# Kernel optimization log

Measured on AMD Instinct MI355X. Metric: run time of the kernel, lower is better.

Reference implementation:

```python
import jax, jax.numpy as jnp
import numpy as np

B, N, C = 2, 2048, 1024
H = 16
R = 4
MLP = 4096
LORA_SCALE = 1.0 / R  # lora_alpha=1, r=4
EPS = 1e-5


def _ln(x, g, b):
    m = jnp.mean(x, axis=-1, keepdims=True)
    v = jnp.mean(jnp.square(x - m), axis=-1, keepdims=True)
    return (x - m) * jax.lax.rsqrt(v + EPS) * g + b


def setup_inputs() -> dict:
    key = jax.random.key(0)
    ks = jax.random.split(key, 16)
    s = lambda k, shape, fan: jax.random.normal(k, shape, jnp.float32) * (1.0 / np.sqrt(fan))
    return {
        "x": jax.random.normal(ks[0], (B, N, C), jnp.float32),
        "pos": jax.random.normal(ks[1], (B, N, C), jnp.float32),
        "Wqkv": s(ks[2], (3 * C, C), C),
        "b_qkv": jnp.zeros((3 * C,), jnp.float32),
        "lora_A": s(ks[3], (2 * R, C), C),          # rows 0:R -> q, R:2R -> v
        "lora_B": s(ks[4], (2 * C, R), R) * 0.1,     # rows 0:C -> q, C:2C -> v
        "Wproj": s(ks[5], (C, C), C),
        "b_proj": jnp.zeros((C,), jnp.float32),
        "ln1_g": jnp.ones((C,), jnp.float32),
        "ln1_b": jnp.zeros((C,), jnp.float32),
        "ln2_g": jnp.ones((C,), jnp.float32),
        "ln2_b": jnp.zeros((C,), jnp.float32),
        "W1": s(ks[6], (MLP, C), C),
        "b1": jnp.zeros((MLP,), jnp.float32),
        "W2": s(ks[7], (C, MLP), MLP),
        "b2": jnp.zeros((C,), jnp.float32),
        "idx": 0,
    }


def reference(x, pos, Wqkv, b_qkv, lora_A, lora_B, Wproj, b_proj,
              ln1_g, ln1_b, ln2_g, ln2_b, W1, b1, W2, b2, idx):
    # (dropout layers are identity in eval mode)
    x = x + pos

    # --- attention block: Residual(PreNormDrop(SelfAttention)) ---
    h = _ln(x, ln1_g, ln1_b)                              # [B,N,C]
    qkv = h @ Wqkv.T + b_qkv                              # [B,N,3C]
    # LoRA MergedLinear: low-rank update on q and v thirds only
    after_A = h @ lora_A.T                                # [B,N,2R]
    dq = after_A[..., :R] @ lora_B[:C].T * LORA_SCALE     # [B,N,C]
    dv = after_A[..., R:] @ lora_B[C:].T * LORA_SCALE     # [B,N,C]
    qkv = qkv.at[..., :C].add(dq).at[..., 2 * C:].add(dv)

    Dh = C // H
    q, k, v = [t.reshape(B, N, H, Dh).transpose(0, 2, 1, 3)
               for t in jnp.split(qkv, 3, axis=-1)]       # each [B,H,N,Dh]
    scale = Dh ** -0.5
    attn = jnp.einsum('bhid,bhjd->bhij', q, k) * scale    # [B,H,N,N]
    attn = jax.nn.softmax(attn, axis=-1)
    o = jnp.einsum('bhij,bhjd->bhid', attn, v)            # [B,H,N,Dh]
    o = o.transpose(0, 2, 1, 3).reshape(B, N, C)
    o = o @ Wproj.T + b_proj
    x = x + o

    # --- FFN block: Residual(PreNorm(FeedForward)) ---
    h2 = _ln(x, ln2_g, ln2_b)
    h2 = jax.nn.gelu(h2 @ W1.T + b1, approximate=False)
    h2 = h2 @ W2.T + b2
    return x + h2
```

## Files before the change

### kernel.cpp

```cpp
#include <hip/hip_runtime.h>
#include <hip/hip_bf16.h>
#include <math.h>

typedef __hip_bfloat16 bf16;
typedef __attribute__((ext_vector_type(4))) float f32x4;
typedef __attribute__((ext_vector_type(16))) float f32x16;
typedef __attribute__((ext_vector_type(8))) short s16x8;

__device__ __forceinline__ void async_cp16(void* lds, const void* g) {
    __builtin_amdgcn_global_load_lds((const __attribute__((address_space(1))) void*)g,
                                     (__attribute__((address_space(3))) void*)lds, 16, 0, 0);
}

__device__ __forceinline__ float gelu_fast(float x) {
    float y = 1.5957691216f * (x + 0.044715f * x * x * x);
    float t = __expf(y);
    float th = 1.0f - 2.0f / (t + 1.0f);
    return 0.5f * x * (1.0f + th);
}

__global__ __launch_bounds__(256)
void cvt_all(const float* __restrict__ w0, const float* __restrict__ w1,
             const float* __restrict__ w2, const float* __restrict__ w3,
             bf16* __restrict__ o0, bf16* __restrict__ o1,
             bf16* __restrict__ o2, bf16* __restrict__ o3) {
    int i = blockIdx.x * 256 + threadIdx.x;
    const float* src; bf16* dst; int j = i;
    if (j < 786432)            { src = w0; dst = o0; }
    else if (j < 1048576)      { j -= 786432;  src = w1; dst = o1; }
    else if (j < 2097152)      { j -= 1048576; src = w2; dst = o2; }
    else                       { j -= 2097152; src = w3; dst = o3; }
    float4 v = ((const float4*)src)[j];
    union { bf16 o[4]; uint2 u; } pk;
    pk.o[0] = __float2bfloat16(v.x); pk.o[1] = __float2bfloat16(v.y);
    pk.o[2] = __float2bfloat16(v.z); pk.o[3] = __float2bfloat16(v.w);
    ((uint2*)dst)[j] = pk.u;
}

template <bool ADD>
__global__ __launch_bounds__(256)
void ln_kernel(const float* __restrict__ xin, const float* __restrict__ pos,
               const float* __restrict__ gam, const float* __restrict__ bet,
               float* __restrict__ x1, bf16* __restrict__ hout) {
    const int row = blockIdx.x, tid = threadIdx.x;
    const size_t off = (size_t)row * 1024;
    float4 v = ((const float4*)(xin + off))[tid];
    if constexpr (ADD) {
        float4 p = ((const float4*)(pos + off))[tid];
        v.x += p.x; v.y += p.y; v.z += p.z; v.w += p.w;
        ((float4*)(x1 + off))[tid] = v;
    }
    float s  = v.x + v.y + v.z + v.w;
    float s2 = v.x*v.x + v.y*v.y + v.z*v.z + v.w*v.w;
#pragma unroll
    for (int o = 32; o >= 1; o >>= 1) { s += __shfl_xor(s, o); s2 += __shfl_xor(s2, o); }
    __shared__ float sS[4], sS2[4];
    int w = tid >> 6, lane = tid & 63;
    if (lane == 0) { sS[w] = s; sS2[w] = s2; }
    __syncthreads();
    float mean = (sS[0] + sS[1] + sS[2] + sS[3]) * (1.f / 1024.f);
    float e2   = (sS2[0] + sS2[1] + sS2[2] + sS2[3]) * (1.f / 1024.f);
    float rstd = rsqrtf(e2 - mean * mean + 1e-5f);
    float4 gv = ((const float4*)gam)[tid], bv = ((const float4*)bet)[tid];
    bf16* ho = hout + off + tid * 4;
    ho[0] = __float2bfloat16((v.x - mean) * rstd * gv.x + bv.x);
    ho[1] = __float2bfloat16((v.y - mean) * rstd * gv.y + bv.y);
    ho[2] = __float2bfloat16((v.z - mean) * rstd * gv.z + bv.z);
    ho[3] = __float2bfloat16((v.w - mean) * rstd * gv.w + bv.w);
}

template <int MODE>
__global__ __launch_bounds__(256)
void gemm_bk64(const bf16* __restrict__ A, const bf16* __restrict__ B,
               const float* __restrict__ bias, bf16* __restrict__ outp,
               int M, int N, int K, int gx) {
    __shared__ bf16 As[2][128 * 64];
    __shared__ bf16 Bs[2][128 * 64];
    const int tid = threadIdx.x;
    const int lane = tid & 63, w = tid >> 6;
    const int grp = lane >> 4, c16 = lane & 15;
    const int wm = (w & 1) * 64, wn = (w >> 1) * 64;
    const int nwg = gridDim.x, bid = blockIdx.x;
    const int sw = (bid & 7) * (nwg >> 3) + (bid >> 3);
    const int bm = (sw / gx) * 128, bn = (sw % gx) * 128;

    f32x4 acc[4][4];
    const f32x4 zero = {0.f, 0.f, 0.f, 0.f};
#pragma unroll
    for (int mi = 0; mi < 4; mi++)
#pragma unroll
        for (int ni = 0; ni < 4; ni++) acc[mi][ni] = zero;

#define STAGE128(bufi, k0)                                                          \
    {                                                                               \
        const int buf_ = (bufi);                                                    \
        const int koff_ = (k0);                                                     \
        _Pragma("unroll") for (int t_ = 0; t_ < 4; t_++) {                          \
            int s_ = t_ * 256 + tid;                                                \
            int row_ = s_ >> 3, db_ = s_ & 7;                                       \
            int gb_ = (db_ ^ (row_ & 7)) << 3;                                      \
            async_cp16(&As[buf_][s_ * 8], A + (size_t)(bm + row_) * K + koff_ + gb_); \
            async_cp16(&Bs[buf_][s_ * 8], B + (size_t)(bn + row_) * K + koff_ + gb_); \
        }                                                                           \
    }

#define COMPUTE128(bufi)                                                            \
    {                                                                               \
        const int buf_ = (bufi);                                                    \
        _Pragma("unroll") for (int kc_ = 0; kc_ < 2; kc_++) {                       \
            s16x8 af_[4], bfv_[4];                                                  \
            _Pragma("unroll") for (int mi_ = 0; mi_ < 4; mi_++) {                   \
                int r_ = wm + mi_ * 16 + c16;                                       \
                af_[mi_] = *(const s16x8*)&As[buf_][r_ * 64 + ((((kc_ << 2) | grp) ^ (r_ & 7)) << 3)]; \
            }                                                                       \
            _Pragma("unroll") for (int ni_ = 0; ni_ < 4; ni_++) {                   \
                int r_ = wn + ni_ * 16 + c16;                                       \
                bfv_[ni_] = *(const s16x8*)&Bs[buf_][r_ * 64 + ((((kc_ << 2) | grp) ^ (r_ & 7)) << 3)]; \
            }                                                                       \
            _Pragma("unroll") for (int mi_ = 0; mi_ < 4; mi_++)                     \
                _Pragma("unroll") for (int ni_ = 0; ni_ < 4; ni_++)                 \
                    acc[mi_][ni_] = __builtin_amdgcn_mfma_f32_16x16x32_bf16(af_[mi_], bfv_[ni_], acc[mi_][ni_], 0, 0, 0); \
        }                                                                           \
    }

    STAGE128(0, 0);
    __syncthreads();
    const int nk = K >> 6;
    int cur = 0;
    for (int t = 0; t < nk - 1; t++) {
        STAGE128(cur ^ 1, (t + 1) << 6);
        COMPUTE128(cur);
        __syncthreads();
        cur ^= 1;
    }
    COMPUTE128(cur);

#undef STAGE128
#undef COMPUTE128

#pragma unroll
    for (int mi = 0; mi < 4; mi++)
#pragma unroll
        for (int ni = 0; ni < 4; ni++) {
            int r0 = bm + wm + mi * 16 + grp * 4;
            int c  = bn + wn + ni * 16 + c16;
            float bv = bias[c];
#pragma unroll
            for (int q = 0; q < 4; q++) {
                size_t idx = (size_t)(r0 + q) * N + c;
                float v = acc[mi][ni][q] + bv;
                if constexpr (MODE == 2) v = gelu_fast(v);
                outp[idx] = __float2bfloat16(v);
            }
        }
}

__global__ __launch_bounds__(256)
void gemm_n64(const bf16* __restrict__ A, const bf16* __restrict__ B,
              const float* __restrict__ bias, const float* __restrict__ resid,
              float* __restrict__ outp, int M, int N, int K, int gx) {
    __shared__ bf16 As[3][128 * 64];
    __shared__ bf16 Bs[3][64 * 64];
    const int tid = threadIdx.x;
    const int lane = tid & 63, w = tid >> 6;
    const int grp = lane >> 4, c16 = lane & 15;
    const int wm = w * 32;
    const int nwg = gridDim.x, bid = blockIdx.x;
    const int sw = (bid & 7) * (nwg >> 3) + (bid >> 3);
    const int bm = (sw / gx) * 128, bn = (sw % gx) * 64;

    f32x4 acc[2][4];
    const f32x4 zero = {0.f, 0.f, 0.f, 0.f};
#pragma unroll
    for (int mi = 0; mi < 2; mi++)
#pragma unroll
        for (int ni = 0; ni < 4; ni++) acc[mi][ni] = zero;

#define STAGE64(bufi, k0)                                                           \
    {                                                                               \
        const int buf_ = (bufi);                                                    \
        const int koff_ = (k0);                                                     \
        _Pragma("unroll") for (int t_ = 0; t_ < 4; t_++) {                          \
            int s_ = t_ * 256 + tid;                                                \
            int row_ = s_ >> 3, db_ = s_ & 7;                                       \
            async_cp16(&As[buf_][s_ * 8], A + (size_t)(bm + row_) * K + koff_ + ((db_ ^ (row_ & 7)) << 3)); \
        }                                                                           \
        _Pragma("unroll") for (int t_ = 0; t_ < 2; t_++) {                          \
            int s_ = t_ * 256 + tid;                                                \
            int row_ = s_ >> 3, db_ = s_ & 7;                                       \
            async_cp16(&Bs[buf_][s_ * 8], B + (size_t)(bn + row_) * K + koff_ + ((db_ ^ (row_ & 7)) << 3)); \
        }                                                                           \
    }

#define COMPUTE64(bufi)                                                             \
    {                                                                               \
        const int buf_ = (bufi);                                                    \
        _Pragma("unroll") for (int kc_ = 0; kc_ < 2; kc_++) {                       \
            s16x8 af_[2], bfv_[4];                                                  \
            _Pragma("unroll") for (int mi_ = 0; mi_ < 2; mi_++) {                   \
                int r_ = wm + mi_ * 16 + c16;                                       \
                af_[mi_] = *(const s16x8*)&As[buf_][r_ * 64 + ((((kc_ << 2) | grp) ^ (r_ & 7)) << 3)]; \
            }                                                                       \
            _Pragma("unroll") for (int ni_ = 0; ni_ < 4; ni_++) {                   \
                int rb_ = ni_ * 16 + c16;                                           \
                bfv_[ni_] = *(const s16x8*)&Bs[buf_][rb_ * 64 + ((((kc_ << 2) | grp) ^ (rb_ & 7)) << 3)]; \
            }                                                                       \
            _Pragma("unroll") for (int mi_ = 0; mi_ < 2; mi_++)                     \
                _Pragma("unroll") for (int ni_ = 0; ni_ < 4; ni_++)                 \
                    acc[mi_][ni_] = __builtin_amdgcn_mfma_f32_16x16x32_bf16(af_[mi_], bfv_[ni_], acc[mi_][ni_], 0, 0, 0); \
        }                                                                           \
    }

#define WAITV12 asm volatile("s_waitcnt vmcnt(12)" ::: "memory")
#define WAITV6  asm volatile("s_waitcnt vmcnt(6)"  ::: "memory")
#define WAITV0  asm volatile("s_waitcnt vmcnt(0)"  ::: "memory")

#define STEP64(BQ, TQ)                                                              \
    {                                                                               \
        const int tq_ = (TQ);                                                       \
        COMPUTE64(BQ);                                                              \
        __builtin_amdgcn_s_barrier();            \
        if (tq_ + 3 < nk) { STAGE64(BQ, (tq_ + 3) << 6); WAITV12; }                 \
        else if (tq_ + 2 < nk) { WAITV6; }                                          \
        else { WAITV0; }                                \
        __builtin_amdgcn_s_barrier();             \
    }

    const int nk = K >> 6;
    STAGE64(0, 0);
    STAGE64(1, 64);
    STAGE64(2, 128);
    WAITV12;
    __builtin_amdgcn_s_barrier();

    for (int t = 0; t < nk - 1; t += 3) {
        STEP64(0, t);
        STEP64(1, t + 1);
        STEP64(2, t + 2);
    }
    COMPUTE64(0);

#undef STEP64
#undef WAITV12
#undef WAITV6
#undef WAITV0
#undef STAGE64
#undef COMPUTE64

#pragma unroll
    for (int mi = 0; mi < 2; mi++)
#pragma unroll
        for (int ni = 0; ni < 4; ni++) {
            int r0 = bm + wm + mi * 16 + grp * 4;
            int c  = bn + ni * 16 + c16;
            float bv = bias[c];
#pragma unroll
            for (int q = 0; q < 4; q++) {
                size_t idx = (size_t)(r0 + q) * N + c;
                outp[idx] = acc[mi][ni][q] + bv + resid[idx];
            }
        }
}

__global__ __launch_bounds__(256)
void lora_a_kernel(const bf16* __restrict__ h, const float* __restrict__ A,
                   float* __restrict__ afterA) {
    const int row = blockIdx.x, tid = threadIdx.x;
    float hv[4];
#pragma unroll
    for (int t = 0; t < 4; t++) hv[t] = __bfloat162float(h[(size_t)row * 1024 + tid * 4 + t]);
    float p[8];
#pragma unroll
    for (int r = 0; r < 8; r++) {
        float4 av = ((const float4*)(A + (size_t)r * 1024))[tid];
        p[r] = hv[0] * av.x + hv[1] * av.y + hv[2] * av.z + hv[3] * av.w;
    }
#pragma unroll
    for (int r = 0; r < 8; r++)
#pragma unroll
        for (int o = 32; o >= 1; o >>= 1) p[r] += __shfl_xor(p[r], o);
    __shared__ float red[4][8];
    int w = tid >> 6, lane = tid & 63;
    if (lane == 0) {
#pragma unroll
        for (int r = 0; r < 8; r++) red[w][r] = p[r];
    }
    __syncthreads();
    if (tid < 8) afterA[(size_t)row * 8 + tid] = red[0][tid] + red[1][tid] + red[2][tid] + red[3][tid];
}

__global__ __launch_bounds__(256)
void attn_prep(const bf16* __restrict__ qkv, const float* __restrict__ afterA,
               const float* __restrict__ loraB, bf16* __restrict__ Qb,
               bf16* __restrict__ Kb, bf16* __restrict__ Vt) {
    const int bh = blockIdx.y, b = bh >> 4, h = bh & 15;
    const int it = blockIdx.x;
    __shared__ bf16 Vs[64 * 65];
    const int tid = threadIdx.x;
#pragma unroll
    for (int t = 0; t < 16; t++) {
        int s = t * 256 + tid;
        int il = s >> 6, d = s & 63;
        int ig = b * 2048 + it * 64 + il;
        size_t grow = (size_t)ig * 3072 + h * 64 + d;
        int col = h * 64 + d;
        const float* aA = afterA + (size_t)ig * 8;
        float4 bq = ((const float4*)loraB)[col];
        float4 bvv = ((const float4*)loraB)[1024 + col];
        float dq = (aA[0]*bq.x  + aA[1]*bq.y  + aA[2]*bq.z  + aA[3]*bq.w)  * 0.25f;
        float dv = (aA[4]*bvv.x + aA[5]*bvv.y + aA[6]*bvv.z + aA[7]*bvv.w) * 0.25f;
        float q = (__bfloat162float(qkv[grow]) + dq) * 0.18033688011f;
        float k = __bfloat162float(qkv[grow + 1024]);
        float v = __bfloat162float(qkv[grow + 2048]) + dv;
        size_t orow = (size_t)(bh * 2048 + it * 64 + il) * 64 + d;
        Qb[orow] = __float2bfloat16(q);
        Kb[orow] = __float2bfloat16(k);
        Vs[d * 65 + il] = __float2bfloat16(v);
    }
    __syncthreads();
#pragma unroll
    for (int t = 0; t < 16; t++) {
        int s = t * 256 + tid;
        int d = s >> 6, il = s & 63;
        Vt[(size_t)(bh * 64 + d) * 2048 + it * 64 + il] = Vs[d * 65 + il];
    }
}

__global__ __launch_bounds__(256)
void attn_fused(const bf16* __restrict__ Qb, const bf16* __restrict__ Kb,
                const bf16* __restrict__ Vt, bf16* __restrict__ Og) {
    __shared__ bf16 Qs[128 * 64], Ks[2][64 * 64], Vs[2][64 * 64];
    const int tid = threadIdx.x;
    const int lane = tid & 63, w = tid >> 6;
    const int c32 = lane & 31, l5 = lane >> 5;
    const int bid = blockIdx.x;
    const int sw = (bid & 7) * 64 + (bid >> 3);
    const int bh = sw >> 4, b = bh >> 4, h = bh & 15;
    const int i0 = (sw & 15) * 128;
    const int rowperm = (c32 & 19) | (((c32 >> 3) & 1) << 2) | (((c32 >> 2) & 1) << 3);

    const size_t qbase = (size_t)(bh * 2048 + i0) * 64;
    const size_t kbase = (size_t)bh * 2048 * 64;
    const size_t vbase = (size_t)bh * 64 * 2048;

#define STAGEKV(bufi, jv)                                                           \
    {                                                                               \
        const int buf_ = (bufi);                                                    \
        const int joff_ = (jv);                                                     \
        _Pragma("unroll") for (int t_ = 0; t_ < 2; t_++) {                          \
            int s_ = t_ * 256 + tid;                                                \
            int row_ = s_ >> 3, db_ = s_ & 7;                                       \
            int gb_ = (db_ ^ (row_ & 7)) << 3;                                      \
            async_cp16(&Ks[buf_][s_ * 8], Kb + kbase + (size_t)(joff_ + row_) * 64 + gb_); \
            async_cp16(&Vs[buf_][s_ * 8], Vt + vbase + (size_t)row_ * 2048 + joff_ + gb_); \
        }                                                                           \
    }

#pragma unroll
    for (int t = 0; t < 4; t++) {
        int s = t * 256 + tid;
        int row = s >> 3, db = s & 7;
        async_cp16(&Qs[s * 8], Qb + qbase + row * 64 + ((db ^ (row & 7)) << 3));
    }
    STAGEKV(0, 0);
    __syncthreads();

    s16x8 qf[4];
    {
        int rq = w * 32 + c32;
#pragma unroll
        for (int kc = 0; kc < 4; kc++) {
            int db = 2 * kc + l5;
            qf[kc] = *(const s16x8*)&Qs[rq * 64 + ((db ^ (rq & 7)) << 3)];
        }
    }

    f32x16 Oq[2];
#pragma unroll
    for (int dq = 0; dq < 2; dq++)
#pragma unroll
        for (int r = 0; r < 16; r++) Oq[dq][r] = 0.f;
    float l_lane = 0.f;

#define ATILE(BUF, JN)                                                              \
    {                                                                               \
        const int jn_ = (JN);                                                       \
        if (jn_ < 32) { STAGEKV((BUF) ^ 1, jn_ << 6); }                             \
        f32x16 Sq[2];                                                               \
        __builtin_amdgcn_s_setprio(1);                                              \
        _Pragma("unroll") for (int jq_ = 0; jq_ < 2; jq_++) {                       \
            _Pragma("unroll") for (int r_ = 0; r_ < 16; r_++) Sq[jq_][r_] = 0.f;    \
            int rk_ = jq_ * 32 + rowperm;                                           \
            _Pragma("unroll") for (int kc_ = 0; kc_ < 4; kc_++) {                   \
                int db_ = 2 * kc_ + l5;                                             \
                s16x8 af_ = *(const s16x8*)&Ks[BUF][rk_ * 64 + ((db_ ^ (rk_ & 7)) << 3)]; \
                Sq[jq_] = __builtin_amdgcn_mfma_f32_32x32x16_bf16(af_, qf[kc_], Sq[jq_], 0, 0, 0); \
            }                                                                       \
        }                                                                           \
        __builtin_amdgcn_s_setprio(0);                                              \
        s16x8 pf_[4];                                                               \
        _Pragma("unroll") for (int kc_ = 0; kc_ < 4; kc_++) {                       \
            union { s16x8 v; unsigned u4[4]; } u_;                                  \
            _Pragma("unroll") for (int pr_ = 0; pr_ < 4; pr_++) {                   \
                float a_ = Sq[kc_ >> 1][8 * (kc_ & 1) + 2 * pr_];                   \
                float b_ = Sq[kc_ >> 1][8 * (kc_ & 1) + 2 * pr_ + 1];               \
                float pa_, pb_;                                                     \
                asm("v_exp_f32 %0, %1" : "=v"(pa_) : "v"(a_));                      \
                asm("v_exp_f32 %0, %1" : "=v"(pb_) : "v"(b_));                      \
                l_lane += pa_; l_lane += pb_;                                       \
                unsigned pk_;                                                       \
                asm("v_cvt_pk_bf16_f32 %0, %1, %2" : "=v"(pk_) : "v"(pa_), "v"(pb_)); \
                u_.u4[pr_] = pk_;                                                   \
            }                                                                       \
            pf_[kc_] = u_.v;                                                        \
        }                                                                           \
        __builtin_amdgcn_s_setprio(1);                                              \
        _Pragma("unroll") for (int dq_ = 0; dq_ < 2; dq_++) {                       \
            int rd_ = dq_ * 32 + c32;                                               \
            _Pragma("unroll") for (int kc_ = 0; kc_ < 4; kc_++) {                   \
                int jb_ = 2 * kc_ + l5;                                             \
                s16x8 af_ = *(const s16x8*)&Vs[BUF][rd_ * 64 + ((jb_ ^ (rd_ & 7)) << 3)]; \
                Oq[dq_] = __builtin_amdgcn_mfma_f32_32x32x16_bf16(af_, pf_[kc_], Oq[dq_], 0, 0, 0); \
            }                                                                       \
        }                                                                           \
        __builtin_amdgcn_s_setprio(0);                                              \
        __syncthreads();                                                            \
    }

    for (int jt = 0; jt < 32; jt += 2) {
        ATILE(0, jt + 1);
        ATILE(1, jt + 2);
    }
#undef ATILE
#undef STAGEKV

    float l = l_lane + __shfl_xor(l_lane, 32);
    float inv = 1.0f / fmaxf(l, 1e-35f);
    int i = i0 + w * 32 + c32;
    size_t obase = (size_t)(b * 2048 + i) * 1024 + h * 64;
#pragma unroll
    for (int dq = 0; dq < 2; dq++)
#pragma unroll
        for (int rg = 0; rg < 4; rg++) {
            union { bf16 e[4]; uint2 u; } pk;
#pragma unroll
            for (int c = 0; c < 4; c++)
                pk.e[c] = __float2bfloat16(Oq[dq][rg * 4 + c] * inv);
            int d0 = dq * 32 + l5 * 4 + rg * 8;
            *(uint2*)&Og[obase + d0] = pk.u;
        }
}

extern "C" void kernel_launch(void* const* d_in, const int* in_sizes, int n_in,
                              void* d_out, int out_size, void* d_ws, size_t ws_size,
                              hipStream_t stream) {
    const float* x     = (const float*)d_in[0];
    const float* pos   = (const float*)d_in[1];
    const float* Wqkv  = (const float*)d_in[2];
    const float* bqkv  = (const float*)d_in[3];
    const float* loraA = (const float*)d_in[4];
    const float* loraB = (const float*)d_in[5];
    const float* Wproj = (const float*)d_in[6];
    const float* bproj = (const float*)d_in[7];
    const float* ln1g  = (const float*)d_in[8];
    const float* ln1b  = (const float*)d_in[9];
    const float* ln2g  = (const float*)d_in[10];
    const float* ln2b  = (const float*)d_in[11];
    const float* W1    = (const float*)d_in[12];
    const float* b1    = (const float*)d_in[13];
    const float* W2    = (const float*)d_in[14];
    const float* b2    = (const float*)d_in[15];

    char* ws = (char*)d_ws;
    float* x1     = (float*)(ws + 0);
    bf16*  hbuf   = (bf16*) (ws + 16777216);
    bf16*  qkv    = (bf16*) (ws + 25165824);
    bf16*  gbuf   = (bf16*) (ws + 50331648);
    float* afterA = (float*)(ws + 83886080);
    bf16*  Qb     = (bf16*) (ws + 84017152);
    bf16*  Kb     = (bf16*) (ws + 92405760);
    bf16*  Vt     = (bf16*) (ws + 100794368);
    bf16*  Obf    = (bf16*) (ws + 109182976);
    bf16*  Wqkvb  = (bf16*) (ws + 117571584);
    bf16*  Wprojb = (bf16*) (ws + 123863040);
    bf16*  W1b    = (bf16*) (ws + 125960192);
    bf16*  W2b    = (bf16*) (ws + 134348800);

    cvt_all<<<12288, 256, 0, stream>>>(Wqkv, Wproj, W1, W2, Wqkvb, Wprojb, W1b, W2b);

    ln_kernel<true><<<4096, 256, 0, stream>>>(x, pos, ln1g, ln1b, x1, hbuf);

    gemm_bk64<0><<<768, 256, 0, stream>>>(hbuf, Wqkvb, bqkv, qkv, 4096, 3072, 1024, 24);

    lora_a_kernel<<<4096, 256, 0, stream>>>(hbuf, loraA, afterA);

    attn_prep<<<dim3(32, 32), 256, 0, stream>>>(qkv, afterA, loraB, Qb, Kb, Vt);
    attn_fused<<<512, 256, 0, stream>>>(Qb, Kb, Vt, Obf);

    gemm_n64<<<512, 256, 0, stream>>>(Obf, Wprojb, bproj, x1, x1, 4096, 1024, 1024, 16);

    ln_kernel<false><<<4096, 256, 0, stream>>>(x1, nullptr, ln2g, ln2b, nullptr, hbuf);

    gemm_bk64<2><<<1024, 256, 0, stream>>>(hbuf, W1b, b1, gbuf, 4096, 4096, 1024, 32);

    gemm_n64<<<512, 256, 0, stream>>>(gbuf, W2b, b2, x1, (float*)d_out, 4096, 1024, 4096, 16);

    (void)in_sizes; (void)n_in; (void)out_size; (void)ws_size;
}
```

Before: 383.8 us.

## Triple-buffer bf16 GEMM with 512-thread blocks and explicit vmcnt waits

The QKV and FFN-up GEMM kernel now runs 8 waves per block, each covering a 64x32 sub-tile instead of 64x64, and cycles through three LDS stages instead of two. Loads are issued three tiles ahead, and explicit s_waitcnt vmcnt counts plus raw s_barrier replace the __syncthreads double-buffer loop. The goal is better hiding of global-to-LDS latency and more waves available to interleave MFMA work. In exchange, LDS use rises to 96KB per block, which likely caps each CU at one block, and each step now has two barriers.

```diff
diff --git a/kernel.cpp b/kernel.cpp
--- a/kernel.cpp
+++ b/kernel.cpp
@@ -70,33 +70,33 @@
 }
 
 template <int MODE>
-__global__ __launch_bounds__(256)
+__global__ __launch_bounds__(512)
 void gemm_bk64(const bf16* __restrict__ A, const bf16* __restrict__ B,
                const float* __restrict__ bias, bf16* __restrict__ outp,
                int M, int N, int K, int gx) {
-    __shared__ bf16 As[2][128 * 64];
-    __shared__ bf16 Bs[2][128 * 64];
+    __shared__ bf16 As[3][128 * 64];
+    __shared__ bf16 Bs[3][128 * 64];
     const int tid = threadIdx.x;
     const int lane = tid & 63, w = tid >> 6;
     const int grp = lane >> 4, c16 = lane & 15;
-    const int wm = (w & 1) * 64, wn = (w >> 1) * 64;
+    const int wm = (w & 1) * 64, wn = (w >> 1) * 32;
     const int nwg = gridDim.x, bid = blockIdx.x;
     const int sw = (bid & 7) * (nwg >> 3) + (bid >> 3);
     const int bm = (sw / gx) * 128, bn = (sw % gx) * 128;
 
-    f32x4 acc[4][4];
+    f32x4 acc[4][2];
     const f32x4 zero = {0.f, 0.f, 0.f, 0.f};
 #pragma unroll
     for (int mi = 0; mi < 4; mi++)
 #pragma unroll
-        for (int ni = 0; ni < 4; ni++) acc[mi][ni] = zero;
+        for (int ni = 0; ni < 2; ni++) acc[mi][ni] = zero;
 
 #define STAGE128(bufi, k0)                                                          \
     {                                                                               \
         const int buf_ = (bufi);                                                    \
         const int koff_ = (k0);                                                     \
-        _Pragma("unroll") for (int t_ = 0; t_ < 4; t_++) {                          \
-            int s_ = t_ * 256 + tid;                                                \
+        _Pragma("unroll") for (int t_ = 0; t_ < 2; t_++) {                          \
+            int s_ = t_ * 512 + tid;                                                \
             int row_ = s_ >> 3, db_ = s_ & 7;                                       \
             int gb_ = (db_ ^ (row_ & 7)) << 3;                                      \
             async_cp16(&As[buf_][s_ * 8], A + (size_t)(bm + row_) * K + koff_ + gb_); \
@@ -108,40 +108,61 @@
     {                                                                               \
         const int buf_ = (bufi);                                                    \
         _Pragma("unroll") for (int kc_ = 0; kc_ < 2; kc_++) {                       \
-            s16x8 af_[4], bfv_[4];                                                  \
+            s16x8 af_[4], bfv_[2];                                                  \
             _Pragma("unroll") for (int mi_ = 0; mi_ < 4; mi_++) {                   \
                 int r_ = wm + mi_ * 16 + c16;                                       \
                 af_[mi_] = *(const s16x8*)&As[buf_][r_ * 64 + ((((kc_ << 2) | grp) ^ (r_ & 7)) << 3)]; \
             }                                                                       \
-            _Pragma("unroll") for (int ni_ = 0; ni_ < 4; ni_++) {                   \
+            _Pragma("unroll") for (int ni_ = 0; ni_ < 2; ni_++) {                   \
                 int r_ = wn + ni_ * 16 + c16;                                       \
                 bfv_[ni_] = *(const s16x8*)&Bs[buf_][r_ * 64 + ((((kc_ << 2) | grp) ^ (r_ & 7)) << 3)]; \
             }                                                                       \
             _Pragma("unroll") for (int mi_ = 0; mi_ < 4; mi_++)                     \
-                _Pragma("unroll") for (int ni_ = 0; ni_ < 4; ni_++)                 \
+                _Pragma("unroll") for (int ni_ = 0; ni_ < 2; ni_++)                 \
                     acc[mi_][ni_] = __builtin_amdgcn_mfma_f32_16x16x32_bf16(af_[mi_], bfv_[ni_], acc[mi_][ni_], 0, 0, 0); \
         }                                                                           \
     }
 
+#define WAITV8 asm volatile("s_waitcnt vmcnt(8)" ::: "memory")
+#define WAITV4 asm volatile("s_waitcnt vmcnt(4)" ::: "memory")
+#define WAITV0 asm volatile("s_waitcnt vmcnt(0)" ::: "memory")
+
+#define STEP128(BQ, TQ)                                                             \
+    {                                                                               \
+        const int tq_ = (TQ);                                                       \
+        COMPUTE128(BQ);                                                             \
+        __builtin_amdgcn_s_barrier();            \
+        if (tq_ + 3 < nk) { STAGE128(BQ, (tq_ + 3) << 6); WAITV8; }                 \
+        else if (tq_ + 2 < nk) { WAITV4; }                                          \
+        else { WAITV0; }                                \
+        __builtin_amdgcn_s_barrier();             \
+    }
+
+    const int nk = K >> 6;
     STAGE128(0, 0);
-    __syncthreads();
-    const int nk = K >> 6;
-    int cur = 0;
-    for (int t = 0; t < nk - 1; t++) {
-        STAGE128(cur ^ 1, (t + 1) << 6);
-        COMPUTE128(cur);
-        __syncthreads();
-        cur ^= 1;
-    }
-    COMPUTE128(cur);
-
+    STAGE128(1, 64);
+    STAGE128(2, 128);
+    WAITV8;
+    __builtin_amdgcn_s_barrier();
+
+    for (int t = 0; t < nk - 1; t += 3) {
+        STEP128(0, t);
+        STEP128(1, t + 1);
+        STEP128(2, t + 2);
+    }
+    COMPUTE128(0);
+
+#undef STEP128
+#undef WAITV8
+#undef WAITV4
+#undef WAITV0
 #undef STAGE128
 #undef COMPUTE128
 
 #pragma unroll
     for (int mi = 0; mi < 4; mi++)
 #pragma unroll
-        for (int ni = 0; ni < 4; ni++) {
+        for (int ni = 0; ni < 2; ni++) {
             int r0 = bm + wm + mi * 16 + grp * 4;
             int c  = bn + wn + ni * 16 + c16;
             float bv = bias[c];
@@ -490,7 +511,7 @@
 
     ln_kernel<true><<<4096, 256, 0, stream>>>(x, pos, ln1g, ln1b, x1, hbuf);
 
-    gemm_bk64<0><<<768, 256, 0, stream>>>(hbuf, Wqkvb, bqkv, qkv, 4096, 3072, 1024, 24);
+    gemm_bk64<0><<<768, 512, 0, stream>>>(hbuf, Wqkvb, bqkv, qkv, 4096, 3072, 1024, 24);
 
     lora_a_kernel<<<4096, 256, 0, stream>>>(hbuf, loraA, afterA);
 
@@ -501,7 +522,7 @@
 
     ln_kernel<false><<<4096, 256, 0, stream>>>(x1, nullptr, ln2g, ln2b, nullptr, hbuf);
 
-    gemm_bk64<2><<<1024, 256, 0, stream>>>(hbuf, W1b, b1, gbuf, 4096, 4096, 1024, 32);
+    gemm_bk64<2><<<1024, 512, 0, stream>>>(hbuf, W1b, b1, gbuf, 4096, 4096, 1024, 32);
 
     gemm_n64<<<512, 256, 0, stream>>>(gbuf, W2b, b2, x1, (float*)d_out, 4096, 1024, 4096, 16);
 
```

Result: slower. 391.5 us (+2.0%).

## Enlarge bf16 GEMM tiles to 256x256 with 512 threads and deeper prefetch

Applied to the files above, without the earlier changes.

The bk64 GEMM used for the QKV projection and FFN1 now computes a 256x256 output tile per block with 8 waves, each wave owning a 128x64 sub-tile. The K loop is restructured so two 64-wide K tiles are kept in flight, using explicit vmcnt waits and raw barriers instead of a single-stage prefetch with __syncthreads. The aim is more operand reuse per LDS load and fewer global reloads of A and B. In exchange, LDS use grows to 128KB per block, so only one block fits per CU. Grids shrink to 192 and 256 blocks, which may leave some CUs idle on the QKV GEMM.

```diff
diff --git a/kernel.cpp b/kernel.cpp
--- a/kernel.cpp
+++ b/kernel.cpp
@@ -70,33 +70,33 @@
 }
 
 template <int MODE>
-__global__ __launch_bounds__(256)
+__global__ __launch_bounds__(512, 2)
 void gemm_bk64(const bf16* __restrict__ A, const bf16* __restrict__ B,
                const float* __restrict__ bias, bf16* __restrict__ outp,
                int M, int N, int K, int gx) {
-    __shared__ bf16 As[2][128 * 64];
-    __shared__ bf16 Bs[2][128 * 64];
+    __shared__ bf16 As[2][256 * 64];
+    __shared__ bf16 Bs[2][256 * 64];
     const int tid = threadIdx.x;
     const int lane = tid & 63, w = tid >> 6;
     const int grp = lane >> 4, c16 = lane & 15;
-    const int wm = (w & 1) * 64, wn = (w >> 1) * 64;
+    const int wm = (w & 1) * 128, wn = (w >> 1) * 64;
     const int nwg = gridDim.x, bid = blockIdx.x;
     const int sw = (bid & 7) * (nwg >> 3) + (bid >> 3);
-    const int bm = (sw / gx) * 128, bn = (sw % gx) * 128;
-
-    f32x4 acc[4][4];
+    const int bm = (sw / gx) * 256, bn = (sw % gx) * 256;
+
+    f32x4 acc[8][4];
     const f32x4 zero = {0.f, 0.f, 0.f, 0.f};
 #pragma unroll
-    for (int mi = 0; mi < 4; mi++)
+    for (int mi = 0; mi < 8; mi++)
 #pragma unroll
         for (int ni = 0; ni < 4; ni++) acc[mi][ni] = zero;
 
-#define STAGE128(bufi, k0)                                                          \
+#define STAGE256(bufi, k0)                                                          \
     {                                                                               \
         const int buf_ = (bufi);                                                    \
         const int koff_ = (k0);                                                     \
         _Pragma("unroll") for (int t_ = 0; t_ < 4; t_++) {                          \
-            int s_ = t_ * 256 + tid;                                                \
+            int s_ = t_ * 512 + tid;                                                \
             int row_ = s_ >> 3, db_ = s_ & 7;                                       \
             int gb_ = (db_ ^ (row_ & 7)) << 3;                                      \
             async_cp16(&As[buf_][s_ * 8], A + (size_t)(bm + row_) * K + koff_ + gb_); \
@@ -104,12 +104,12 @@
         }                                                                           \
     }
 
-#define COMPUTE128(bufi)                                                            \
+#define COMPUTE256(bufi)                                                            \
     {                                                                               \
         const int buf_ = (bufi);                                                    \
         _Pragma("unroll") for (int kc_ = 0; kc_ < 2; kc_++) {                       \
-            s16x8 af_[4], bfv_[4];                                                  \
-            _Pragma("unroll") for (int mi_ = 0; mi_ < 4; mi_++) {                   \
+            s16x8 af_[8], bfv_[4];                                                  \
+            _Pragma("unroll") for (int mi_ = 0; mi_ < 8; mi_++) {                   \
                 int r_ = wm + mi_ * 16 + c16;                                       \
                 af_[mi_] = *(const s16x8*)&As[buf_][r_ * 64 + ((((kc_ << 2) | grp) ^ (r_ & 7)) << 3)]; \
             }                                                                       \
@@ -117,29 +117,46 @@
                 int r_ = wn + ni_ * 16 + c16;                                       \
                 bfv_[ni_] = *(const s16x8*)&Bs[buf_][r_ * 64 + ((((kc_ << 2) | grp) ^ (r_ & 7)) << 3)]; \
             }                                                                       \
-            _Pragma("unroll") for (int mi_ = 0; mi_ < 4; mi_++)                     \
+            _Pragma("unroll") for (int mi_ = 0; mi_ < 8; mi_++)                     \
                 _Pragma("unroll") for (int ni_ = 0; ni_ < 4; ni_++)                 \
                     acc[mi_][ni_] = __builtin_amdgcn_mfma_f32_16x16x32_bf16(af_[mi_], bfv_[ni_], acc[mi_][ni_], 0, 0, 0); \
         }                                                                           \
     }
 
-    STAGE128(0, 0);
-    __syncthreads();
+#define WAITV8 asm volatile("s_waitcnt vmcnt(8)" ::: "memory")
+#define WAITV0 asm volatile("s_waitcnt vmcnt(0)" ::: "memory")
+
+#define STEP256(BQ, TQ)                                                             \
+    {                                                                               \
+        const int tq_ = (TQ);                                                       \
+        COMPUTE256(BQ);                                                             \
+        __builtin_amdgcn_s_barrier();            \
+        if (tq_ + 2 < nk) { STAGE256(BQ, (tq_ + 2) << 6); WAITV8; }                 \
+        else { WAITV0; }                                \
+        __builtin_amdgcn_s_barrier();             \
+    }
+
     const int nk = K >> 6;
-    int cur = 0;
-    for (int t = 0; t < nk - 1; t++) {
-        STAGE128(cur ^ 1, (t + 1) << 6);
-        COMPUTE128(cur);
-        __syncthreads();
-        cur ^= 1;
-    }
-    COMPUTE128(cur);
-
-#undef STAGE128
-#undef COMPUTE128
-
-#pragma unroll
-    for (int mi = 0; mi < 4; mi++)
+    STAGE256(0, 0);
+    STAGE256(1, 64);
+    WAITV8;
+    __builtin_amdgcn_s_barrier();
+
+    for (int t = 0; t < nk - 2; t += 2) {
+        STEP256(0, t);
+        STEP256(1, t + 1);
+    }
+    STEP256(0, nk - 2);
+    COMPUTE256(1);
+
+#undef STEP256
+#undef WAITV8
+#undef WAITV0
+#undef STAGE256
+#undef COMPUTE256
+
+#pragma unroll
+    for (int mi = 0; mi < 8; mi++)
 #pragma unroll
         for (int ni = 0; ni < 4; ni++) {
             int r0 = bm + wm + mi * 16 + grp * 4;
@@ -490,7 +507,7 @@
 
     ln_kernel<true><<<4096, 256, 0, stream>>>(x, pos, ln1g, ln1b, x1, hbuf);
 
-    gemm_bk64<0><<<768, 256, 0, stream>>>(hbuf, Wqkvb, bqkv, qkv, 4096, 3072, 1024, 24);
+    gemm_bk64<0><<<192, 512, 0, stream>>>(hbuf, Wqkvb, bqkv, qkv, 4096, 3072, 1024, 12);
 
     lora_a_kernel<<<4096, 256, 0, stream>>>(hbuf, loraA, afterA);
 
@@ -501,7 +518,7 @@
 
     ln_kernel<false><<<4096, 256, 0, stream>>>(x1, nullptr, ln2g, ln2b, nullptr, hbuf);
 
-    gemm_bk64<2><<<1024, 256, 0, stream>>>(hbuf, W1b, b1, gbuf, 4096, 4096, 1024, 32);
+    gemm_bk64<2><<<256, 512, 0, stream>>>(hbuf, W1b, b1, gbuf, 4096, 4096, 1024, 16);
 
     gemm_n64<<<512, 256, 0, stream>>>(gbuf, W2b, b2, x1, (float*)d_out, 4096, 1024, 4096, 16);
 
```

Measured after the change: 370.2 us. -3.5%, faster.
